# Performance work log

Measured on AMD Instinct MI355X. Metric: run time of the kernel, lower is better.

The kernel has to match this reference:

```python
import jax, jax.numpy as jnp
import numpy as np

B, N, E, H = 1, 4096, 2048, 16
D = E // H  # head_size = 128
DEGREE = 4
LN_EPS = 1e-5
ROPE_BASE = 10000.0


def rope_cos_sin(n, d):
    # [n, d//2] tables
    inv_freq = 1.0 / (ROPE_BASE ** (jnp.arange(0, d, 2, dtype=jnp.float32) / d))
    t = jnp.arange(n, dtype=jnp.float32)[:, None] * inv_freq[None, :]
    return jnp.cos(t), jnp.sin(t)


def apply_rope(x, cos, sin):
    # x: [b, n, h, d]; rotate-half RoPE
    x1, x2 = jnp.split(x, 2, axis=-1)
    c = cos[None, :, None, :]
    s = sin[None, :, None, :]
    return jnp.concatenate([x1 * c - x2 * s, x1 * s + x2 * c], axis=-1)


def layernorm(x, scale, bias, eps=LN_EPS):
    m = jnp.mean(x, axis=-1, keepdims=True)
    v = jnp.var(x, axis=-1, keepdims=True)
    return (x - m) * jax.lax.rsqrt(v + eps) * scale + bias


def polynomial_attention(q, k, v, degree, is_causal):
    # q,k,v: [b, h, n, d]
    a = jnp.einsum('bhnd,bhmd->bhnm', q, k) ** degree
    if is_causal:
        a = jnp.tril(a)
    denom = jnp.sum(a, axis=-1, keepdims=True)
    return jnp.einsum('bhnm,bhmd->bhnd', a / denom, v)


def setup_inputs() -> dict:
    key = jax.random.key(0)
    k0, k1, k2 = jax.random.split(key, 3)
    x = jax.random.normal(k0, (B, N, E), dtype=jnp.float32)
    # Dense(3*emb_dim, use_bias=False) and Dense(emb_dim, use_bias=False)
    w_qkv = jax.random.normal(k1, (E, 3 * E), dtype=jnp.float32) * (1.0 / np.sqrt(E))
    w_out = jax.random.normal(k2, (E, E), dtype=jnp.float32) * (1.0 / np.sqrt(E))
    # shared pre-attention LayerNorm over head dim (flax init: scale=1, bias=0)
    ln_scale = jnp.ones((D,), dtype=jnp.float32)
    ln_bias = jnp.zeros((D,), dtype=jnp.float32)
    return {"x": x, "w_qkv": w_qkv, "w_out": w_out,
            "ln_scale": ln_scale, "ln_bias": ln_bias}


def reference(x, w_qkv, w_out, ln_scale, ln_bias):
    b, n, e = x.shape
    proj = x @ w_qkv                              # [b, n, 3e]
    q, k, v = jnp.split(proj, 3, axis=-1)
    q = q.reshape(b, n, H, D)
    k = k.reshape(b, n, H, D)
    v = v.reshape(b, n, H, D)
    cos, sin = rope_cos_sin(n, D)
    q = apply_rope(q, cos, sin)
    k = apply_rope(k, cos, sin)
    # transpose branch (non-softmax): [b, h, n, d]
    q = q.transpose(0, 2, 1, 3)
    k = k.transpose(0, 2, 1, 3)
    v = v.transpose(0, 2, 1, 3)
    # shared pre_attn LayerNorm applied to q and k
    q = layernorm(q, ln_scale, ln_bias)
    k = layernorm(k, ln_scale, ln_bias)
    out = polynomial_attention(q, k, v, DEGREE, True)  # [b, h, n, d]
    out = out.transpose(0, 2, 1, 3).reshape(b, n, e)
    out = out @ w_out                              # dropout rate 0 / inference: identity
    return out
```

## Files before the change

kernel.cpp:

```cpp
#include <hip/hip_runtime.h>
#include <stdint.h>
#include <math.h>

#define N_SEQ 4096
#define EDIM  2048
#define NH    16
#define HD    128

typedef __attribute__((ext_vector_type(8))) short bf16x8;
typedef __attribute__((ext_vector_type(4))) float f32x4;

#define AS1 __attribute__((address_space(1)))
#define AS3 __attribute__((address_space(3)))

__device__ __forceinline__ void gll16(const unsigned short* g, unsigned short* l) {
    __builtin_amdgcn_global_load_lds((const AS1 unsigned int*)g,
                                     (AS3 unsigned int*)l, 16, 0, 0);
}

__device__ __forceinline__ unsigned short f2bf(float f) {
    union { float f; unsigned u; } v; v.f = f;
    unsigned r = v.u + 0x7FFFu + ((v.u >> 16) & 1u);
    return (unsigned short)(r >> 16);
}
__device__ __forceinline__ float bf2f(unsigned short h) {
    union { unsigned u; float f; } v; v.u = ((unsigned)h) << 16;
    return v.f;
}

__global__ void k_convert_x(const float* __restrict__ x,
                            unsigned short* __restrict__ xb, int n4) {
    int i = blockIdx.x * blockDim.x + threadIdx.x;
    int stride = gridDim.x * blockDim.x;
    for (; i < n4; i += stride) {
        float4 v = ((const float4*)x)[i];
        ushort4 o;
        o.x = f2bf(v.x); o.y = f2bf(v.y); o.z = f2bf(v.z); o.w = f2bf(v.w);
        ((ushort4*)xb)[i] = o;
    }
}

__global__ void k_transpose_f32_bf16(const float* __restrict__ in,
                                     unsigned short* __restrict__ out,
                                     int R, int C) {
    __shared__ unsigned short Ls[64][68];
    const int c0 = blockIdx.x * 64, r0 = blockIdx.y * 64;
    const int t = threadIdx.x;
    #pragma unroll
    for (int i = 0; i < 4; ++i) {
        int ch = i * 256 + t;
        int r = ch >> 4, c4 = (ch & 15) * 4;
        float4 v = *(const float4*)&in[(size_t)(r0 + r) * C + c0 + c4];
        ushort4 o;
        o.x = f2bf(v.x); o.y = f2bf(v.y); o.z = f2bf(v.z); o.w = f2bf(v.w);
        *(ushort4*)&Ls[r][c4] = o;
    }
    __syncthreads();
    #pragma unroll
    for (int i = 0; i < 2; ++i) {
        int ch = i * 256 + t;
        int rr = ch >> 3, c8 = (ch & 7) * 8;
        unsigned short vals[8];
        #pragma unroll
        for (int j = 0; j < 8; ++j) vals[j] = Ls[c8 + j][rr];
        uint4 pk;
        pk.x = (unsigned)vals[0] | ((unsigned)vals[1] << 16);
        pk.y = (unsigned)vals[2] | ((unsigned)vals[3] << 16);
        pk.z = (unsigned)vals[4] | ((unsigned)vals[5] << 16);
        pk.w = (unsigned)vals[6] | ((unsigned)vals[7] << 16);
        *(uint4*)&out[(size_t)(c0 + rr) * R + r0 + c8] = pk;
    }
}

template<int F32OUT>
__launch_bounds__(256, 2)
__global__ void k_gemm_bt(const unsigned short* __restrict__ A,
                          const unsigned short* __restrict__ Bt,
                          void* __restrict__ C,
                          int M, int N, int K) {
    __shared__ unsigned short sh[2 * 128 * 64];
    unsigned short* As = sh;
    unsigned short* Bs = sh + 128 * 64;

    const int t = threadIdx.x;
    const int wave = t >> 6, lane = t & 63;
    const int wm = wave >> 1, wn = wave & 1;
    const int lg = lane >> 4, lr = lane & 15;

    const int nbx = gridDim.x;
    const int nwg = nbx * gridDim.y;
    int bid = blockIdx.y * nbx + blockIdx.x;
    int swz = (bid & 7) * (nwg >> 3) + (bid >> 3);
    const int m0 = (swz / nbx) * 128;
    const int n0 = (swz % nbx) * 128;

    const unsigned short* aptr = A  + (size_t)m0 * K;
    const unsigned short* bptr = Bt + (size_t)n0 * K;

    f32x4 acc[4][4];
    #pragma unroll
    for (int i = 0; i < 4; ++i)
        #pragma unroll
        for (int j = 0; j < 4; ++j) acc[i][j] = f32x4{0.f, 0.f, 0.f, 0.f};

    int schr[4], srow[4], scb[4];
    #pragma unroll
    for (int i = 0; i < 4; ++i) {
        int ch = (i * 4 + wave) * 64 + lane;
        schr[i] = ch;
        srow[i] = ch >> 3;
        scb[i]  = (ch & 7) ^ ((ch >> 3) & 7);
    }

    const int nkb = K >> 6;
    for (int kb = 0; kb < nkb; ++kb) {
        __syncthreads();
        #pragma unroll
        for (int i = 0; i < 4; ++i) {
            const size_t goff = (size_t)srow[i] * K + (size_t)kb * 64 + scb[i] * 8;
            gll16(&aptr[goff], &As[schr[i] * 8]);
            gll16(&bptr[goff], &Bs[schr[i] * 8]);
        }
        __syncthreads();

        #pragma unroll
        for (int kk = 0; kk < 2; ++kk) {
            bf16x8 af[4], bf[4];
            const int cbx = ((kk * 4 + lg) ^ (lr & 7)) * 8;
            #pragma unroll
            for (int i = 0; i < 4; ++i) {
                af[i] = *(const bf16x8*)&As[(wm * 64 + i * 16 + lr) * 64 + cbx];
                bf[i] = *(const bf16x8*)&Bs[(wn * 64 + i * 16 + lr) * 64 + cbx];
            }
            #pragma unroll
            for (int i = 0; i < 4; ++i)
                #pragma unroll
                for (int j = 0; j < 4; ++j)
                    acc[i][j] = __builtin_amdgcn_mfma_f32_16x16x32_bf16(af[i], bf[j], acc[i][j], 0, 0, 0);
        }
    }

    if (F32OUT) {
        #pragma unroll
        for (int i = 0; i < 4; ++i) {
            int row0 = m0 + wm * 64 + i * 16 + lg * 4;
            #pragma unroll
            for (int j = 0; j < 4; ++j) {
                int col = n0 + wn * 64 + j * 16 + lr;
                #pragma unroll
                for (int r = 0; r < 4; ++r)
                    ((float*)C)[(size_t)(row0 + r) * N + col] = acc[i][j][r];
            }
        }
    } else {
        __syncthreads();
        unsigned short* Cs = sh;
        #pragma unroll
        for (int i = 0; i < 4; ++i) {
            #pragma unroll
            for (int j = 0; j < 4; ++j) {
                int col = wn * 64 + j * 16 + lr;
                #pragma unroll
                for (int r = 0; r < 4; ++r)
                    Cs[(wm * 64 + i * 16 + lg * 4 + r) * 128 + col] = f2bf(acc[i][j][r]);
            }
        }
        __syncthreads();
        #pragma unroll
        for (int i = 0; i < 8; ++i) {
            int ch = i * 256 + t;
            int row = ch >> 4, c8 = (ch & 15) * 8;
            *(uint4*)&((unsigned short*)C)[(size_t)(m0 + row) * N + n0 + c8] =
                *(const uint4*)&Cs[row * 128 + c8];
        }
    }
}

__global__ void k_ropeln(const unsigned short* __restrict__ proj,
                         const float* __restrict__ ln_scale,
                         const float* __restrict__ ln_bias,
                         unsigned short* __restrict__ Qh,
                         unsigned short* __restrict__ Kh) {
    const int n = blockIdx.x;
    const int wave = threadIdx.x >> 6, lane = threadIdx.x & 63;
    float inv = expf(-((float)(2 * lane) / 128.0f) * 9.210340371976184f);
    float ang = (float)n * inv;
    float c = cosf(ang), s = sinf(ang);
    const float sc1 = ln_scale[lane], sc2 = ln_scale[lane + 64];
    const float b1 = ln_bias[lane],  b2 = ln_bias[lane + 64];

    for (int r = wave; r < 32; r += 4) {
        int h = r >> 1, qk = r & 1;
        const unsigned short* src = proj + (size_t)n * (3 * EDIM) + qk * EDIM + h * HD;
        float x1 = bf2f(src[lane]), x2 = bf2f(src[lane + 64]);
        float o1 = x1 * c - x2 * s;
        float o2 = x1 * s + x2 * c;
        float sum = o1 + o2, sq = o1 * o1 + o2 * o2;
        #pragma unroll
        for (int d = 1; d < 64; d <<= 1) {
            sum += __shfl_xor(sum, d);
            sq  += __shfl_xor(sq, d);
        }
        float mean = sum * (1.0f / 128.0f);
        float var = sq * (1.0f / 128.0f) - mean * mean;
        float rstd = rsqrtf(var + 1e-5f);
        float y1 = (o1 - mean) * rstd * sc1 + b1;
        float y2 = (o2 - mean) * rstd * sc2 + b2;
        unsigned short* dst = (qk ? Kh : Qh) + ((size_t)h * N_SEQ + n) * HD;
        dst[lane]      = f2bf(y1);
        dst[lane + 64] = f2bf(y2);
    }
}

__global__ void k_vtrans(const unsigned short* __restrict__ proj,
                         unsigned short* __restrict__ Vt) {
    __shared__ unsigned short Ls[64][136];
    const int h = blockIdx.y;
    const int n0 = blockIdx.x * 64;
    const int t = threadIdx.x;
    #pragma unroll
    for (int i = 0; i < 4; ++i) {
        int ch = i * 256 + t;
        int r = ch >> 4, d0 = (ch & 15) * 8;
        uint4 v = *(const uint4*)&proj[(size_t)(n0 + r) * (3 * EDIM) + 2 * EDIM + h * HD + d0];
        *(uint4*)&Ls[r][d0] = v;
    }
    __syncthreads();
    #pragma unroll
    for (int i = 0; i < 4; ++i) {
        int ch = i * 256 + t;
        int d = ch >> 3, nb = (ch & 7) * 8;
        unsigned short vals[8];
        #pragma unroll
        for (int j = 0; j < 8; ++j) vals[j] = Ls[nb + j][d];
        uint4 pk;
        pk.x = (unsigned)vals[0] | ((unsigned)vals[1] << 16);
        pk.y = (unsigned)vals[2] | ((unsigned)vals[3] << 16);
        pk.z = (unsigned)vals[4] | ((unsigned)vals[5] << 16);
        pk.w = (unsigned)vals[6] | ((unsigned)vals[7] << 16);
        *(uint4*)&Vt[((size_t)h * HD + d) * N_SEQ + n0 + nb] = pk;
    }
}

__launch_bounds__(256, 2)
__global__ void k_attn(const unsigned short* __restrict__ Qh,
                       const unsigned short* __restrict__ Kh,
                       const unsigned short* __restrict__ Vt,
                       unsigned short* __restrict__ O) {
    __shared__ unsigned short pool[5 * 8192];

    const int t = threadIdx.x;
    const int w = t >> 6, lane = t & 63;
    const int lg = lane >> 4, lr = lane & 15;

    const int s = blockIdx.x & 255;
    const int batch = blockIdx.x >> 8;
    const int x = s & 7;
    const int hb = (s >> 3) & 1;
    const int h = x * 2 + hb;
    const int qq = s >> 4;
    const int qb = batch ? qq : (31 - qq);
    const int q0 = qb * 128;
    const int qbase = q0 + w * 32;

    bf16x8 qf[2][4];
    #pragma unroll
    for (int mi = 0; mi < 2; ++mi)
        #pragma unroll
        for (int kk = 0; kk < 4; ++kk)
            qf[mi][kk] = *(const bf16x8*)&Qh[((size_t)h * N_SEQ + qbase + mi * 16 + lr) * HD + kk * 32 + lg * 8];

    f32x4 acc[2][8];
    #pragma unroll
    for (int i = 0; i < 2; ++i)
        #pragma unroll
        for (int j = 0; j < 8; ++j) acc[i][j] = f32x4{0.f, 0.f, 0.f, 0.f};
    f32x4 accd[2];
    accd[0] = f32x4{0.f, 0.f, 0.f, 0.f};
    accd[1] = f32x4{0.f, 0.f, 0.f, 0.f};

    bf16x8 onesf;
    {
        short ov = (lr == 0) ? (short)0x3F80 : (short)0;
        #pragma unroll
        for (int j = 0; j < 8; ++j) onesf[j] = ov;
    }

    int kch[4], vch[4];
    const unsigned short* kg[4];
    const unsigned short* vg[4];
    #pragma unroll
    for (int i = 0; i < 4; ++i) {
        int ch = i * 256 + t;
        kch[i] = ch;
        int r = ch >> 4, p = ch & 15;
        int csrc = (p & 8) | ((p ^ r) & 7);
        kg[i] = Kh + ((size_t)h * N_SEQ + r) * HD + csrc * 8;
    }
    #pragma unroll
    for (int i = 0; i < 4; ++i) {
        int ch = i * 256 + t;
        vch[i] = ch;
        int d = ch >> 3, p2 = ch & 7;
        int c2src = (p2 ^ d) & 7;
        vg[i] = Vt + ((size_t)h * HD + d) * N_SEQ + c2src * 8;
    }

    const int nkb = 2 * qb + 2;

    {
        #pragma unroll
        for (int i = 0; i < 4; ++i) { gll16(kg[i], pool + kch[i] * 8); kg[i] += 64 * HD; }
        #pragma unroll
        for (int i = 0; i < 4; ++i) { gll16(vg[i], pool + 16384 + vch[i] * 8); vg[i] += 64; }
    }

    unsigned short* Pw = pool + 32768 + w * 2048;

    for (int kb = 0; kb < nkb; ++kb) {
        const int cur = kb & 1;
        const int k0 = kb * 64;

        if (kb + 1 < nkb) {
            const int nxt = cur ^ 1;
            unsigned short* Kn = pool + nxt * 8192;
            unsigned short* Vn = pool + 16384 + nxt * 8192;
            #pragma unroll
            for (int i = 0; i < 4; ++i) { gll16(kg[i], Kn + kch[i] * 8); kg[i] += 64 * HD; }
            #pragma unroll
            for (int i = 0; i < 4; ++i) { gll16(vg[i], Vn + vch[i] * 8); vg[i] += 64; }
            asm volatile("s_waitcnt vmcnt(8)" ::: "memory");
        } else {
            asm volatile("s_waitcnt vmcnt(0)" ::: "memory");
        }
        __builtin_amdgcn_s_barrier();

        const unsigned short* Kc = pool + cur * 8192;
        const unsigned short* Vc = pool + 16384 + cur * 8192;

        f32x4 sa[2][4];
        #pragma unroll
        for (int i = 0; i < 2; ++i)
            #pragma unroll
            for (int j = 0; j < 4; ++j) sa[i][j] = f32x4{0.f, 0.f, 0.f, 0.f};
        #pragma unroll
        for (int nn = 0; nn < 2; ++nn) {
            bf16x8 kf[2][4];
            #pragma unroll
            for (int nj = 0; nj < 2; ++nj)
                #pragma unroll
                for (int kk = 0; kk < 4; ++kk) {
                    int row = (nn * 2 + nj) * 16 + lr;
                    int c = kk * 4 + lg;
                    int cs = (c & 8) | ((c ^ row) & 7);
                    kf[nj][kk] = *(const bf16x8*)&Kc[row * 128 + cs * 8];
                }
            #pragma unroll
            for (int kk = 0; kk < 4; ++kk)
                #pragma unroll
                for (int nj = 0; nj < 2; ++nj)
                    #pragma unroll
                    for (int mi = 0; mi < 2; ++mi)
                        sa[mi][nn * 2 + nj] = __builtin_amdgcn_mfma_f32_16x16x32_bf16(
                            qf[mi][kk], kf[nj][kk], sa[mi][nn * 2 + nj], 0, 0, 0);
        }

        const bool nomask = (k0 + 63 <= qbase);
        #pragma unroll
        for (int mi = 0; mi < 2; ++mi)
            #pragma unroll
            for (int ni = 0; ni < 4; ++ni) {
                int gk = k0 + ni * 16 + lr;
                #pragma unroll
                for (int r = 0; r < 4; ++r) {
                    int rw = mi * 16 + lg * 4 + r;
                    float sv = sa[mi][ni][r];
                    float t2 = sv * sv;
                    float p = t2 * t2;
                    if (!nomask) p = (gk <= qbase + rw) ? p : 0.0f;
                    int ci = ni * 2 + (lr >> 3);
                    int cs = (ci ^ (rw & 7)) & 7;
                    Pw[rw * 64 + cs * 8 + (lr & 7)] = f2bf(p);
                }
            }

        #pragma unroll
        for (int kk = 0; kk < 2; ++kk) {
            bf16x8 pf[2];
            #pragma unroll
            for (int mi = 0; mi < 2; ++mi) {
                int row = mi * 16 + lr;
                int cs = ((kk * 4 + lg) ^ (row & 7)) & 7;
                pf[mi] = *(const bf16x8*)&Pw[row * 64 + cs * 8];
            }
            #pragma unroll
            for (int ni = 0; ni < 8; ++ni) {
                int row = ni * 16 + lr;
                int cs2 = ((kk * 4 + lg) ^ (row & 7)) & 7;
                bf16x8 vf = *(const bf16x8*)&Vc[row * 64 + cs2 * 8];
                #pragma unroll
                for (int mi = 0; mi < 2; ++mi)
                    acc[mi][ni] = __builtin_amdgcn_mfma_f32_16x16x32_bf16(pf[mi], vf, acc[mi][ni], 0, 0, 0);
            }
            #pragma unroll
            for (int mi = 0; mi < 2; ++mi)
                accd[mi] = __builtin_amdgcn_mfma_f32_16x16x32_bf16(pf[mi], onesf, accd[mi], 0, 0, 0);
        }

        __builtin_amdgcn_s_barrier();
    }

    unsigned short* Cs = pool;
    #pragma unroll
    for (int mi = 0; mi < 2; ++mi) {
        #pragma unroll
        for (int r = 0; r < 4; ++r) {
            float dv = __shfl(accd[mi][r], lane & 48);
            float rinv = 1.0f / dv;
            int rw = w * 32 + mi * 16 + lg * 4 + r;
            #pragma unroll
            for (int ni = 0; ni < 8; ++ni)
                Cs[rw * 128 + ni * 16 + lr] = f2bf(acc[mi][ni][r] * rinv);
        }
    }
    __syncthreads();
    #pragma unroll
    for (int i = 0; i < 8; ++i) {
        int ch = i * 256 + t;
        int row = ch >> 4, c8 = (ch & 15) * 8;
        *(uint4*)&O[(size_t)(q0 + row) * EDIM + h * HD + c8] = *(const uint4*)&Cs[row * 128 + c8];
    }
}

extern "C" void kernel_launch(void* const* d_in, const int* in_sizes, int n_in,
                              void* d_out, int out_size, void* d_ws, size_t ws_size,
                              hipStream_t stream) {
    const float* x        = (const float*)d_in[0];
    const float* w_qkv    = (const float*)d_in[1];
    const float* w_out    = (const float*)d_in[2];
    const float* ln_scale = (const float*)d_in[3];
    const float* ln_bias  = (const float*)d_in[4];

    if (ws_size < 134217728u) return;

    char* ws = (char*)d_ws;
    unsigned short* xb    = (unsigned short*)(ws);
    unsigned short* wqkvT = (unsigned short*)(ws + 16777216);
    unsigned short* woutT = (unsigned short*)(ws + 41943040);
    unsigned short* proj  = (unsigned short*)(ws + 50331648);
    unsigned short* Kh    = (unsigned short*)(ws + 100663296);
    unsigned short* Vt    = (unsigned short*)(ws + 117440512);
    unsigned short* Qh    = wqkvT;
    unsigned short* attnO = xb;

    k_convert_x<<<2048, 256, 0, stream>>>(x, xb, (N_SEQ * EDIM) / 4);
    k_transpose_f32_bf16<<<dim3(3 * EDIM / 64, EDIM / 64), 256, 0, stream>>>(w_qkv, wqkvT, EDIM, 3 * EDIM);
    k_transpose_f32_bf16<<<dim3(EDIM / 64, EDIM / 64), 256, 0, stream>>>(w_out, woutT, EDIM, EDIM);
    k_gemm_bt<0><<<dim3(3 * EDIM / 128, N_SEQ / 128), 256, 0, stream>>>(xb, wqkvT, proj, N_SEQ, 3 * EDIM, EDIM);
    k_ropeln<<<N_SEQ, 256, 0, stream>>>(proj, ln_scale, ln_bias, Qh, Kh);
    k_vtrans<<<dim3(N_SEQ / 64, NH), 256, 0, stream>>>(proj, Vt);
    k_attn<<<512, 256, 0, stream>>>(Qh, Kh, Vt, attnO);
    k_gemm_bt<1><<<dim3(EDIM / 128, N_SEQ / 128), 256, 0, stream>>>(attnO, woutT, (float*)d_out, N_SEQ, EDIM, EDIM);
}
```

Measured before the change: 325.0 us.

## Keep attention P tile in registers via swapped-operand MFMA, dropping LDS round trip

Swaps the operand order of the QK^T MFMA so each lane holds transposed scores, letting P be packed into bf16 registers with v_cvt_pk_bf16_f32 and fed directly as the A operand of the PV MFMA. This removes the per-wave LDS staging buffer for P, its stores and reloads, and the shared-memory pool shrinks accordingly, which may help occupancy. V fragments are now gathered as two 8-byte LDS reads to match the new k ordering. It also wraps the MFMA blocks in s_setprio to favour matrix issue.

```diff
diff --git a/kernel.cpp b/kernel.cpp
--- a/kernel.cpp
+++ b/kernel.cpp
@@ -247,7 +247,7 @@
                        const unsigned short* __restrict__ Kh,
                        const unsigned short* __restrict__ Vt,
                        unsigned short* __restrict__ O) {
-    __shared__ unsigned short pool[5 * 8192];
+    __shared__ unsigned short pool[4 * 8192];
 
     const int t = threadIdx.x;
     const int w = t >> 6, lane = t & 63;
@@ -315,7 +315,7 @@
         for (int i = 0; i < 4; ++i) { gll16(vg[i], pool + 16384 + vch[i] * 8); vg[i] += 64; }
     }
 
-    unsigned short* Pw = pool + 32768 + w * 2048;
+    union U8 { unsigned u[4]; bf16x8 v; };
 
     for (int kb = 0; kb < nkb; ++kb) {
         const int cur = kb & 1;
@@ -355,6 +355,7 @@
                     int cs = (c & 8) | ((c ^ row) & 7);
                     kf[nj][kk] = *(const bf16x8*)&Kc[row * 128 + cs * 8];
                 }
+            __builtin_amdgcn_s_setprio(1);
             #pragma unroll
             for (int kk = 0; kk < 4; ++kk)
                 #pragma unroll
@@ -362,49 +363,63 @@
                     #pragma unroll
                     for (int mi = 0; mi < 2; ++mi)
                         sa[mi][nn * 2 + nj] = __builtin_amdgcn_mfma_f32_16x16x32_bf16(
-                            qf[mi][kk], kf[nj][kk], sa[mi][nn * 2 + nj], 0, 0, 0);
-        }
-
+                            kf[nj][kk], qf[mi][kk], sa[mi][nn * 2 + nj], 0, 0, 0);
+            __builtin_amdgcn_s_setprio(0);
+        }
+
+        unsigned wreg[2][4][2];
         const bool nomask = (k0 + 63 <= qbase);
         #pragma unroll
         for (int mi = 0; mi < 2; ++mi)
             #pragma unroll
-            for (int ni = 0; ni < 4; ++ni) {
-                int gk = k0 + ni * 16 + lr;
+            for (int nj = 0; nj < 4; ++nj) {
+                float p[4];
                 #pragma unroll
                 for (int r = 0; r < 4; ++r) {
-                    int rw = mi * 16 + lg * 4 + r;
-                    float sv = sa[mi][ni][r];
+                    float sv = sa[mi][nj][r];
                     float t2 = sv * sv;
-                    float p = t2 * t2;
-                    if (!nomask) p = (gk <= qbase + rw) ? p : 0.0f;
-                    int ci = ni * 2 + (lr >> 3);
-                    int cs = (ci ^ (rw & 7)) & 7;
-                    Pw[rw * 64 + cs * 8 + (lr & 7)] = f2bf(p);
+                    p[r] = t2 * t2;
+                    if (!nomask) {
+                        int gk = k0 + nj * 16 + lg * 4 + r;
+                        int gq = qbase + mi * 16 + lr;
+                        p[r] = (gk <= gq) ? p[r] : 0.0f;
+                    }
                 }
-            }
-
-        #pragma unroll
-        for (int kk = 0; kk < 2; ++kk) {
-            bf16x8 pf[2];
+                asm("v_cvt_pk_bf16_f32 %0, %1, %2" : "=v"(wreg[mi][nj][0]) : "v"(p[0]), "v"(p[1]));
+                asm("v_cvt_pk_bf16_f32 %0, %1, %2" : "=v"(wreg[mi][nj][1]) : "v"(p[2]), "v"(p[3]));
+            }
+
+        #pragma unroll
+        for (int s2 = 0; s2 < 2; ++s2) {
+            bf16x8 pa[2];
             #pragma unroll
             for (int mi = 0; mi < 2; ++mi) {
-                int row = mi * 16 + lr;
-                int cs = ((kk * 4 + lg) ^ (row & 7)) & 7;
-                pf[mi] = *(const bf16x8*)&Pw[row * 64 + cs * 8];
-            }
+                U8 u;
+                u.u[0] = wreg[mi][2 * s2][0];
+                u.u[1] = wreg[mi][2 * s2][1];
+                u.u[2] = wreg[mi][2 * s2 + 1][0];
+                u.u[3] = wreg[mi][2 * s2 + 1][1];
+                pa[mi] = u.v;
+            }
+            __builtin_amdgcn_s_setprio(1);
             #pragma unroll
             for (int ni = 0; ni < 8; ++ni) {
-                int row = ni * 16 + lr;
-                int cs2 = ((kk * 4 + lg) ^ (row & 7)) & 7;
-                bf16x8 vf = *(const bf16x8*)&Vc[row * 64 + cs2 * 8];
+                int d = ni * 16 + lr;
+                int base = d * 64 + (lg & 1) * 4;
+                int cA = ((s2 * 4 + (lg >> 1)) ^ d) & 7;
+                int cB = ((s2 * 4 + 2 + (lg >> 1)) ^ d) & 7;
+                uint2 va = *(const uint2*)&Vc[base + cA * 8];
+                uint2 vb = *(const uint2*)&Vc[base + cB * 8];
+                U8 tv;
+                tv.u[0] = va.x; tv.u[1] = va.y; tv.u[2] = vb.x; tv.u[3] = vb.y;
                 #pragma unroll
                 for (int mi = 0; mi < 2; ++mi)
-                    acc[mi][ni] = __builtin_amdgcn_mfma_f32_16x16x32_bf16(pf[mi], vf, acc[mi][ni], 0, 0, 0);
+                    acc[mi][ni] = __builtin_amdgcn_mfma_f32_16x16x32_bf16(pa[mi], tv.v, acc[mi][ni], 0, 0, 0);
             }
             #pragma unroll
             for (int mi = 0; mi < 2; ++mi)
-                accd[mi] = __builtin_amdgcn_mfma_f32_16x16x32_bf16(pf[mi], onesf, accd[mi], 0, 0, 0);
+                accd[mi] = __builtin_amdgcn_mfma_f32_16x16x32_bf16(pa[mi], onesf, accd[mi], 0, 0, 0);
+            __builtin_amdgcn_s_setprio(0);
         }
 
         __builtin_amdgcn_s_barrier();
```

New measurement: 312.8 us. -3.7%, faster.
